# Kernel optimization log

Hardware: AMD Instinct MI355X
Metric: run time of the kernel (lower is better)

Reference implementation:

```python
import jax, jax.numpy as jnp
import numpy as np

N, T, D_KQ, E_KQ, D_V, E_V, H = 2, 2048, 1024, 1024, 1024, 1024, 16


def setup_inputs() -> dict:
    key = jax.random.key(0)
    ks = jax.random.split(key, 12)
    def lin(k, fan_in, fan_out):
        return jax.random.normal(k, (fan_in, fan_out), jnp.float32) * (1.0 / np.sqrt(fan_in))
    return {
        "kq": jax.random.normal(ks[0], (N, T, D_KQ), jnp.float32),
        "v": jax.random.normal(ks[1], (N, T, D_V), jnp.float32),
        "Wk": lin(ks[2], D_KQ, E_KQ), "bk": jnp.zeros((E_KQ,), jnp.float32),
        "Wq": lin(ks[3], D_KQ, E_KQ), "bq": jnp.zeros((E_KQ,), jnp.float32),
        "Wv": lin(ks[4], D_V, E_V),   "bv": jnp.zeros((E_V,), jnp.float32),
        "W1": lin(ks[5], E_V, 4 * E_V), "b1": jnp.zeros((4 * E_V,), jnp.float32),
        "W2": lin(ks[6], 4 * E_V, E_V), "b2": jnp.zeros((E_V,), jnp.float32),
    }


def _shifted_causal_mask(T):
    # triu(-inf, diagonal=0): block j >= i (strictly-past attention), except [0,0] unmasked
    row = jnp.arange(T)[:, None]
    col = jnp.arange(T)[None, :]
    mask = jnp.where(col < row, 0.0, -jnp.inf).astype(jnp.float32)
    return mask.at[0, 0].set(0.0)


def reference(kq, v, Wk, bk, Wq, bq, Wv, bv, W1, b1, W2, b2):
    n, T, _ = kq.shape
    hd_kq = E_KQ // H
    hd_v = E_V // H
    # projections -> [n, H, T, hd]
    k = (kq @ Wk + bk).reshape(n, T, H, hd_kq).transpose(0, 2, 1, 3)
    q = (kq @ Wq + bq).reshape(n, T, H, hd_kq).transpose(0, 2, 1, 3)
    vv = (v @ Wv + bv).reshape(n, T, H, hd_v).transpose(0, 2, 1, 3)
    # NOTE: no 1/sqrt(d) scaling, faithful to source
    scores = jnp.einsum("bhqd,bhkd->bhqk", q, k) + _shifted_causal_mask(T)
    attn = jax.nn.softmax(scores, axis=-1)
    out = jnp.einsum("bhqk,bhkd->bhqd", attn, vv)
    out = out.transpose(0, 2, 1, 3).reshape(n, T, E_V)
    # GELU FFN (torch nn.GELU default = exact erf form)
    h = jax.nn.gelu(out @ W1 + b1, approximate=False)
    return h @ W2 + b2
```

## Files before the change

kernel.cpp:

```cpp
#include <hip/hip_runtime.h>

typedef short bf16x8 __attribute__((ext_vector_type(8)));
typedef unsigned short u16x8 __attribute__((ext_vector_type(8)));
typedef float f32x4 __attribute__((ext_vector_type(4)));
typedef unsigned short u16;

#define MFMA16(a, b, c) __builtin_amdgcn_mfma_f32_16x16x32_bf16((a), (b), (c), 0, 0, 0)
#define VMCNT0() asm volatile("s_waitcnt vmcnt(0)" ::: "memory")
#define VMCNTN(n) asm volatile("s_waitcnt vmcnt(" #n ")" ::: "memory")

__device__ __forceinline__ u16 bf16_rtn(float f) {
  unsigned u = __float_as_uint(f);
  u += 0x7fffu + ((u >> 16) & 1u);
  return (u16)(u >> 16);
}
__device__ __forceinline__ float bf16_to_f(u16 h) {
  return __uint_as_float(((unsigned)h) << 16);
}
__device__ __forceinline__ void splitf(float f, u16& hi, u16& lo) {
  hi = bf16_rtn(f);
  lo = bf16_rtn(f - bf16_to_f(hi));
}
__device__ __forceinline__ void gload16(const void* g, void* l) {
  __builtin_amdgcn_global_load_lds(
      (const __attribute__((address_space(1))) unsigned int*)g,
      (__attribute__((address_space(3))) unsigned int*)l, 16, 0, 0);
}
__device__ __forceinline__ float exp2_hw(float x) {
  float r;
  asm("v_exp_f32 %0, %1" : "=v"(r) : "v"(x));
  return r;
}
__device__ __forceinline__ float gelu_t(float x) {
  float u = x * x;
  float z2 = x * fmaf(u, 0.10294407f, 2.30222726f);
  float den = exp2_hw(z2) + 1.0f;
  float s = __builtin_amdgcn_rcpf(den);
  return fmaf(-x, s, x);
}
__device__ __forceinline__ void swz_bid(int& bx, int& by) {
  int gx = gridDim.x;
  int lin = (int)blockIdx.y * gx + (int)blockIdx.x;
  int cpx = (gx * (int)gridDim.y) >> 3;
  int nl = (lin & 7) * cpx + (lin >> 3);
  bx = nl % gx;
  by = nl / gx;
}

__global__ void k_cvt(const float* __restrict__ a, const float* __restrict__ b,
                      u16* __restrict__ ah, u16* __restrict__ vb) {
  int i = blockIdx.x * blockDim.x + threadIdx.x;
  const int N4 = 1 << 20;
  const float4 v4 = (i < N4) ? ((const float4*)a)[i] : ((const float4*)b)[i - N4];
  ushort4 h;
  h.x = bf16_rtn(v4.x);
  h.y = bf16_rtn(v4.y);
  h.z = bf16_rtn(v4.z);
  h.w = bf16_rtn(v4.w);
  if (i < N4)
    ((ushort4*)ah)[i] = h;
  else
    ((ushort4*)vb)[i - N4] = h;
}

__global__ void k_tconvW(const float* __restrict__ Wk, const float* __restrict__ Wq,
                         const float* __restrict__ Wv, u16* __restrict__ hi,
                         u16* __restrict__ lo, u16* __restrict__ wvt) {
  int z = blockIdx.z;
  const float* in = (z == 0) ? Wk : (z == 1) ? Wq : Wv;
  __shared__ float tile[32][33];
  int c0 = blockIdx.x * 32, r0 = blockIdx.y * 32;
  int tx = threadIdx.x & 31, ty = threadIdx.x >> 5;
#pragma unroll
  for (int i = 0; i < 4; ++i)
    tile[ty + i * 8][tx] = in[(size_t)(r0 + ty + i * 8) * 1024 + c0 + tx];
  __syncthreads();
#pragma unroll
  for (int i = 0; i < 4; ++i) {
    float v = tile[tx][ty + i * 8];
    size_t o = (size_t)(c0 + ty + i * 8) * 1024 + r0 + tx;
    if (z < 2) {
      u16 h, l;
      splitf(v, h, l);
      hi[(size_t)z * 1048576 + o] = h;
      lo[(size_t)z * 1048576 + o] = l;
    } else {
      wvt[o] = bf16_rtn(v);
    }
  }
}

__global__ void k_tconv(const float* __restrict__ in, u16* __restrict__ hi,
                        int R, int C) {
  __shared__ float tile[32][33];
  int c0 = blockIdx.x * 32, r0 = blockIdx.y * 32;
  int tx = threadIdx.x & 31, ty = threadIdx.x >> 5;
#pragma unroll
  for (int i = 0; i < 4; ++i)
    tile[ty + i * 8][tx] = in[(size_t)(r0 + ty + i * 8) * C + c0 + tx];
  __syncthreads();
#pragma unroll
  for (int i = 0; i < 4; ++i)
    hi[(size_t)(c0 + ty + i * 8) * R + r0 + tx] = bf16_rtn(tile[tx][ty + i * 8]);
}

template <int GELU, int OUT, int BN>
__global__ __launch_bounds__(256) void k_gemm(
    const u16* __restrict__ A, const u16* __restrict__ B,
    const float* __restrict__ bias, void* __restrict__ C0,
    int M, int Nc, int K) {
  const int NB = BN / 32;
  const int BUFE = 8192 + BN * 64;
  __shared__ u16 sm[3 * BUFE];

  int bx, by;
  swz_bid(bx, by);
  int m0 = by * 128, n0 = bx * BN;
  int t = threadIdx.x, lane = t & 63, w = t >> 6;
  int wr = (w >> 1) * 64, wc = (w & 1) * (BN / 2);
  int li = lane & 15, g = lane >> 4;
  int lrow = lane >> 3, lcg = lane & 7;

  f32x4 acc[4][NB] = {};
  const int nk = K >> 6;

  auto stage = [&](int kb, int buf) {
    int k0 = kb * 64;
    u16* base = sm + buf * BUFE;
#pragma unroll
    for (int j = 0; j < 4; ++j) {
      int jj = w * 4 + j;
      int row = jj * 8 + lrow;
      int cg = lcg ^ (row & 7);
      gload16(A + (size_t)(m0 + row) * K + k0 + cg * 8, base + jj * 512);
    }
#pragma unroll
    for (int j = 0; j < NB; ++j) {
      int jj = w * NB + j;
      int row = jj * 8 + lrow;
      int cg = lcg ^ (row & 7);
      gload16(B + (size_t)(n0 + row) * K + k0 + cg * 8, base + 8192 + jj * 512);
    }
  };

  stage(0, 0);
  stage(1, 1);
  if (NB == 4) { VMCNTN(8); } else { VMCNTN(6); }
  __syncthreads();

  int cur = 0;
  for (int kb = 0; kb < nk; ++kb) {
    int stb = cur + 2;
    if (stb >= 3) stb -= 3;
    if (kb + 2 < nk) stage(kb + 2, stb);

    const u16* bs = sm + cur * BUFE;
#pragma unroll
    for (int kk = 0; kk < 2; ++kk) {
      bf16x8 af[4], bf[NB];
#pragma unroll
      for (int i = 0; i < 4; ++i) {
        int row = wr + i * 16 + li;
        af[i] = *(const bf16x8*)&bs[row * 64 + (((kk * 4 + g) ^ (li & 7)) << 3)];
      }
#pragma unroll
      for (int b = 0; b < NB; ++b) {
        int row = wc + b * 16 + li;
        bf[b] = *(const bf16x8*)&bs[8192 + row * 64 + (((kk * 4 + g) ^ (li & 7)) << 3)];
      }
#pragma unroll
      for (int a = 0; a < 4; ++a)
#pragma unroll
        for (int b = 0; b < NB; ++b) acc[a][b] = MFMA16(af[a], bf[b], acc[a][b]);
    }
    if (kb + 2 < nk) {
      if (NB == 4) { VMCNTN(8); } else { VMCNTN(6); }
    } else {
      VMCNT0();
    }
    __syncthreads();
    cur = (cur == 2) ? 0 : cur + 1;
  }

#pragma unroll
  for (int a = 0; a < 4; ++a)
#pragma unroll
    for (int b = 0; b < NB; ++b)
#pragma unroll
      for (int r = 0; r < 4; ++r) {
        int row = m0 + wr + a * 16 + g * 4 + r;
        int col = n0 + wc + b * 16 + li;
        float v = acc[a][b][r] + bias[col];
        if (GELU) v = gelu_t(v);
        if (OUT == 0) {
          ((float*)C0)[(size_t)row * Nc + col] = v;
        } else if (OUT == 1) {
          ((u16*)C0)[(size_t)row * Nc + col] = bf16_rtn(v);
        } else if (OUT == 5) {
          int nn = row >> 11, tt = row & 2047, kbb = tt >> 6, tr = tt & 63;
          int hq = col >> 6, d = col & 63;
          size_t base = (((size_t)nn * 16 + hq) * 32 + kbb) * 8192 + 4096;
          size_t ov = base + d * 64 + (tr & 7) + (((tr >> 3) ^ (d & 7)) << 3);
          ((u16*)C0)[ov] = bf16_rtn(v);
        }
      }
}

template <int GELU, int OUT>
__global__ __launch_bounds__(512, 1) void k_gemm2(
    const u16* __restrict__ A, const u16* __restrict__ B,
    const float* __restrict__ bias, void* __restrict__ C0,
    int M, int Nc, int K) {
  const int BUFE = 32768;
  __shared__ u16 sm[2 * BUFE];

  int bx, by;
  swz_bid(bx, by);
  int m0 = by * 256, n0 = bx * 256;
  int t = threadIdx.x, lane = t & 63, w = t >> 6;
  int wr = (w >> 2) * 128, wc = (w & 3) * 64;
  int li = lane & 15, g = lane >> 4;
  int lrow = lane >> 3, lcg = lane & 7;

  f32x4 acc[8][4] = {};
  const int nk = K >> 6;

  auto stage = [&](int kb, int buf) {
    int k0 = kb * 64;
    u16* base = sm + buf * BUFE;
#pragma unroll
    for (int j = 0; j < 4; ++j) {
      int jj = w * 4 + j;
      int row = jj * 8 + lrow;
      int cg = lcg ^ (row & 7);
      gload16(A + (size_t)(m0 + row) * K + k0 + cg * 8, base + jj * 512);
      gload16(B + (size_t)(n0 + row) * K + k0 + cg * 8, base + 16384 + jj * 512);
    }
  };

  stage(0, 0);
  VMCNT0();
  __syncthreads();

  int cur = 0;
  for (int kb = 0; kb < nk; ++kb) {
    if (kb + 1 < nk) stage(kb + 1, cur ^ 1);

    const u16* bs = sm + cur * BUFE;
#pragma unroll
    for (int kk = 0; kk < 2; ++kk) {
      bf16x8 af[8], bf[4];
#pragma unroll
      for (int i = 0; i < 8; ++i) {
        int row = wr + i * 16 + li;
        af[i] = *(const bf16x8*)&bs[row * 64 + (((kk * 4 + g) ^ (li & 7)) << 3)];
      }
#pragma unroll
      for (int b = 0; b < 4; ++b) {
        int row = wc + b * 16 + li;
        bf[b] = *(const bf16x8*)&bs[16384 + row * 64 + (((kk * 4 + g) ^ (li & 7)) << 3)];
      }
#pragma unroll
      for (int a = 0; a < 8; ++a)
#pragma unroll
        for (int b = 0; b < 4; ++b) acc[a][b] = MFMA16(af[a], bf[b], acc[a][b]);
    }
    VMCNT0();
    __syncthreads();
    cur ^= 1;
  }

#pragma unroll
  for (int a = 0; a < 8; ++a)
#pragma unroll
    for (int b = 0; b < 4; ++b)
#pragma unroll
      for (int r = 0; r < 4; ++r) {
        int row = m0 + wr + a * 16 + g * 4 + r;
        int col = n0 + wc + b * 16 + li;
        float v = acc[a][b][r] + bias[col];
        if (GELU) v = gelu_t(v);
        if (OUT == 1)
          ((u16*)C0)[(size_t)row * Nc + col] = bf16_rtn(v);
        else
          ((float*)C0)[(size_t)row * Nc + col] = v;
      }
}

__global__ __launch_bounds__(256) void k_gemm_s(
    const u16* __restrict__ Ahi, const u16* __restrict__ Bhi,
    const u16* __restrict__ Blo, const float* __restrict__ bias,
    const float* __restrict__ bias2, void* __restrict__ C0,
    void* __restrict__ C1, void* __restrict__ C2, int M, int Nc, int K) {
  const int BUFE = 12288;
  __shared__ u16 sm[3 * BUFE];

  int bx, by;
  swz_bid(bx, by);
  int m0 = by * 128, n0 = bx * 128;
  int t = threadIdx.x, lane = t & 63, w = t >> 6;
  int wr = (w >> 1) * 64, wc = (w & 1) * 64;
  int li = lane & 15, g = lane >> 4;
  int srow = lane >> 2;
  int sc = ((lane & 3) ^ ((srow >> 1) & 3)) * 8;

  f32x4 acc[4][4] = {};
  const int nk = K >> 5;

  auto stage = [&](int kb, int buf) {
    int k0 = kb * 32;
    u16* base = sm + buf * BUFE;
#pragma unroll
    for (int c = 0; c < 2; ++c) {
      int row = w * 32 + c * 16 + srow;
      int ldso = w * 1024 + c * 512;
      gload16(Ahi + (size_t)(m0 + row) * K + k0 + sc, base + ldso);
      gload16(Bhi + (size_t)(n0 + row) * K + k0 + sc, base + 4096 + ldso);
      gload16(Blo + (size_t)(n0 + row) * K + k0 + sc, base + 8192 + ldso);
    }
  };

  stage(0, 0);
  stage(1, 1);
  VMCNTN(6);
  __syncthreads();

  int cur = 0;
  for (int kb = 0; kb < nk; ++kb) {
    int stb = cur + 2;
    if (stb >= 3) stb -= 3;
    if (kb + 2 < nk) stage(kb + 2, stb);

    const u16* bs = sm + cur * BUFE;
    bf16x8 af[4], bfr[4], bfl[4];
#pragma unroll
    for (int i = 0; i < 4; ++i) {
      int swz = (g ^ ((li >> 1) & 3)) << 3;
      af[i] = *(const bf16x8*)&bs[(wr + i * 16 + li) * 32 + swz];
      bfr[i] = *(const bf16x8*)&bs[4096 + (wc + i * 16 + li) * 32 + swz];
      bfl[i] = *(const bf16x8*)&bs[8192 + (wc + i * 16 + li) * 32 + swz];
    }
#pragma unroll
    for (int a = 0; a < 4; ++a)
#pragma unroll
      for (int b = 0; b < 4; ++b) {
        acc[a][b] = MFMA16(af[a], bfr[b], acc[a][b]);
        acc[a][b] = MFMA16(af[a], bfl[b], acc[a][b]);
      }
    if (kb + 2 < nk) {
      VMCNTN(6);
    } else {
      VMCNT0();
    }
    __syncthreads();
    cur = (cur == 2) ? 0 : cur + 1;
  }

#pragma unroll
  for (int a = 0; a < 4; ++a)
#pragma unroll
    for (int b = 0; b < 4; ++b)
#pragma unroll
      for (int r = 0; r < 4; ++r) {
        int row = m0 + wr + a * 16 + g * 4 + r;
        int col = n0 + wc + b * 16 + li;
        float bb = col < 1024 ? bias[col] : bias2[col - 1024];
        float v = acc[a][b][r] + bb;
        if (col < 1024) {
          int nn = row >> 11, tt = row & 2047, kbb = tt >> 6, tr = tt & 63;
          int hq = col >> 6, d = col & 63, ks = d >> 5, dc = d & 31;
          size_t base = (((size_t)nn * 16 + hq) * 32 + kbb) * 8192;
          size_t oh = base + ks * 2048 + tr * 32 + (dc & 7) +
                      (((dc >> 3) ^ ((tr >> 1) & 3)) << 3);
          ((u16*)C0)[oh] = bf16_rtn(v);
        } else {
          int cq = col - 1024;
          float vq = v * 1.4426950408889634f;
          u16 hh, ll;
          splitf(vq, hh, ll);
          size_t off = (((size_t)(row >> 11) * 16 + (cq >> 6)) * 2048 + (row & 2047)) * 64 + (cq & 63);
          ((u16*)C1)[off] = hh;
          ((u16*)C2)[off] = ll;
        }
      }
}

__global__ __launch_bounds__(512) void k_attn(
    const u16* __restrict__ Qh, const u16* __restrict__ Ql,
    const u16* __restrict__ KV, u16* __restrict__ out) {
  const int T = 2048, HD = 64, H = 16, E = 1024;
  int hc = blockIdx.x;
  int h = hc & 15, n = hc >> 4;
  int qq = 15 - (int)blockIdx.y;
  __shared__ u16 KB[3][8192];
  __shared__ u16 P[2][128][36];
  int t = threadIdx.x, lane = t & 63, w = t >> 6;
  int li = lane & 15, g = lane >> 4;

  const size_t nh = (size_t)n * H + h;
  const u16* qhb = Qh + (nh * 2048 + (size_t)qq * 128) * 64;
  const u16* qlb = Ql + (nh * 2048 + (size_t)qq * 128) * 64;
  const u16* kvb = KV + nh * 32 * 8192;

  bf16x8 qh[2], ql[2];
#pragma unroll
  for (int ks = 0; ks < 2; ++ks) {
    qh[ks] = *(const bf16x8*)&qhb[(w * 16 + li) * 64 + ks * 32 + g * 8];
    ql[ks] = *(const bf16x8*)&qlb[(w * 16 + li) * 64 + ks * 32 + g * 8];
  }

#pragma unroll
  for (int j = 0; j < 2; ++j)
    gload16(kvb + (w * 2 + j) * 512 + lane * 8, &KB[0][(w * 2 + j) * 512]);
#pragma unroll
  for (int j = 0; j < 2; ++j)
    gload16(kvb + 8192 + (w * 2 + j) * 512 + lane * 8, &KB[1][(w * 2 + j) * 512]);
  VMCNTN(2);
  __syncthreads();

  float lr[4] = {0.f, 0.f, 0.f, 0.f};
  f32x4 O[4] = {};
  int cur = 0;
  const int nkb = 2 * qq + 2;

  for (int kb = 0; kb < nkb; ++kb) {
    int stb = cur + 2;
    if (stb >= 3) stb -= 3;
    if (kb + 2 < nkb) {
      const u16* src = kvb + (size_t)(kb + 2) * 8192 + (w * 2) * 512 + lane * 8;
#pragma unroll
      for (int j = 0; j < 2; ++j)
        gload16(src + j * 512, &KB[stb][(w * 2 + j) * 512]);
    }

    f32x4 s[4] = {};
#pragma unroll
    for (int ks = 0; ks < 2; ++ks)
#pragma unroll
      for (int c = 0; c < 4; ++c) {
        int jr = c * 16 + li;
        int sw = (jr >> 1) & 3;
        bf16x8 kh = *(const bf16x8*)&KB[cur][ks * 2048 + jr * 32 + ((g ^ sw) << 3)];
        s[c] = MFMA16(qh[ks], kh, s[c]);
        s[c] = MFMA16(ql[ks], kh, s[c]);
      }

    if (kb >= 2 * qq) {
#pragma unroll
      for (int c = 0; c < 4; ++c)
#pragma unroll
        for (int r = 0; r < 4; ++r) {
          int i = qq * 128 + w * 16 + g * 4 + r;
          int j = kb * 64 + c * 16 + li;
          if (!(j < i || (i == 0 && j == 0))) s[c][r] = -INFINITY;
        }
    }

#pragma unroll
    for (int c = 0; c < 4; ++c)
#pragma unroll
      for (int r = 0; r < 4; ++r) {
        float p = exp2_hw(s[c][r]);
        s[c][r] = p;
        lr[r] += p;
      }

#pragma unroll
    for (int c = 0; c < 4; ++c)
#pragma unroll
      for (int r = 0; r < 4; ++r)
        P[c >> 1][w * 16 + g * 4 + r][(c & 1) * 16 + li] = bf16_rtn(s[c][r]);

#pragma unroll
    for (int ks = 0; ks < 2; ++ks) {
      bf16x8 pa = *(const bf16x8*)&P[ks][w * 16 + li][g * 8];
#pragma unroll
      for (int c = 0; c < 4; ++c) {
        int d = c * 16 + li;
        int tc = ks * 4 + g;
        bf16x8 vb = *(const bf16x8*)&KB[cur][4096 + d * 64 + ((tc ^ (d & 7)) << 3)];
        O[c] = MFMA16(pa, vb, O[c]);
      }
    }
    if (kb + 2 < nkb) {
      VMCNTN(2);
    } else {
      VMCNT0();
    }
    __syncthreads();
    cur = (cur == 2) ? 0 : cur + 1;
  }

#pragma unroll
  for (int off = 1; off < 16; off <<= 1)
#pragma unroll
    for (int r = 0; r < 4; ++r) lr[r] += __shfl_xor(lr[r], off, 16);

#pragma unroll
  for (int c = 0; c < 4; ++c)
#pragma unroll
    for (int r = 0; r < 4; ++r) {
      float v = O[c][r] / lr[r];
      size_t row = (size_t)n * T + qq * 128 + w * 16 + g * 4 + r;
      out[row * E + h * HD + c * 16 + li] = bf16_rtn(v);
    }
}

extern "C" void kernel_launch(void* const* d_in, const int* in_sizes, int n_in,
                              void* d_out, int out_size, void* d_ws, size_t ws_size,
                              hipStream_t stream) {
  const float* kq = (const float*)d_in[0];
  const float* v = (const float*)d_in[1];
  const float* Wk = (const float*)d_in[2];
  const float* bk = (const float*)d_in[3];
  const float* Wq = (const float*)d_in[4];
  const float* bq = (const float*)d_in[5];
  const float* Wv = (const float*)d_in[6];
  const float* bv = (const float*)d_in[7];
  const float* W1 = (const float*)d_in[8];
  const float* b1 = (const float*)d_in[9];
  const float* W2 = (const float*)d_in[10];
  const float* b2 = (const float*)d_in[11];
  float* outp = (float*)d_out;

  char* ws = (char*)d_ws;
  u16* kq_hi = (u16*)(ws + 0);
  u16* v_bf = (u16*)(ws + 8388608);
  u16* hbuf = (u16*)(ws + 0);
  u16* WkqT_hi = (u16*)(ws + 33554432);
  u16* WkqT_lo = (u16*)(ws + 37748736);
  u16* WvT = (u16*)(ws + 41943040);
  u16* W1T = (u16*)(ws + 44040192);
  u16* W2T = (u16*)(ws + 52428800);
  u16* Qh = (u16*)(ws + 60817408);
  u16* Ql = (u16*)(ws + 69206016);
  u16* KV = (u16*)(ws + 77594624);
  u16* attn_o = (u16*)(ws + 102760448);

  k_cvt<<<8192, 256, 0, stream>>>(kq, v, kq_hi, v_bf);
  k_tconvW<<<dim3(32, 32, 3), 256, 0, stream>>>(Wk, Wq, Wv, WkqT_hi, WkqT_lo, WvT);
  k_tconv<<<dim3(128, 32), 256, 0, stream>>>(W1, W1T, 1024, 4096);
  k_tconv<<<dim3(32, 128), 256, 0, stream>>>(W2, W2T, 4096, 1024);

  k_gemm_s<<<dim3(16, 32), 256, 0, stream>>>(
      kq_hi, WkqT_hi, WkqT_lo, bk, bq, KV, Qh, Ql, 4096, 2048, 1024);
  k_gemm<0, 5, 64><<<dim3(16, 32), 256, 0, stream>>>(
      v_bf, WvT, bv, KV, 4096, 1024, 1024);

  k_attn<<<dim3(32, 16), 512, 0, stream>>>(Qh, Ql, KV, attn_o);

  k_gemm2<1, 1><<<dim3(16, 16), 512, 0, stream>>>(
      attn_o, W1T, b1, hbuf, 4096, 4096, 1024);
  k_gemm<0, 0, 128><<<dim3(8, 32), 256, 0, stream>>>(
      hbuf, W2T, b2, outp, 4096, 1024, 4096);
}
```

Before: 213.6 us.

## Pair causal query tiles per attention block and merge prep kernels

The attention kernel now processes two query tiles per block (qa=15-y and qb=y). This balances causal work across blocks and lets both tiles reuse each K/V tile loaded into LDS, halving the grid. The four conversion and transpose kernels are merged into a single k_prep launch to cut launch overhead. The cost is higher register and LDS use per attention block, which may reduce occupancy, and only 256 attention blocks remain to fill the device.

New measurement: 217.5 us. Within noise of the previous version (+1.8%).

```diff
diff --git a/kernel.cpp b/kernel.cpp
--- a/kernel.cpp
+++ b/kernel.cpp
@@ -47,61 +47,71 @@
   by = nl / gx;
 }
 
-__global__ void k_cvt(const float* __restrict__ a, const float* __restrict__ b,
-                      u16* __restrict__ ah, u16* __restrict__ vb) {
-  int i = blockIdx.x * blockDim.x + threadIdx.x;
-  const int N4 = 1 << 20;
-  const float4 v4 = (i < N4) ? ((const float4*)a)[i] : ((const float4*)b)[i - N4];
-  ushort4 h;
-  h.x = bf16_rtn(v4.x);
-  h.y = bf16_rtn(v4.y);
-  h.z = bf16_rtn(v4.z);
-  h.w = bf16_rtn(v4.w);
-  if (i < N4)
-    ((ushort4*)ah)[i] = h;
-  else
-    ((ushort4*)vb)[i - N4] = h;
-}
-
-__global__ void k_tconvW(const float* __restrict__ Wk, const float* __restrict__ Wq,
-                         const float* __restrict__ Wv, u16* __restrict__ hi,
-                         u16* __restrict__ lo, u16* __restrict__ wvt) {
-  int z = blockIdx.z;
-  const float* in = (z == 0) ? Wk : (z == 1) ? Wq : Wv;
+__global__ void k_prep(const float* __restrict__ kq, const float* __restrict__ v,
+                       const float* __restrict__ Wk, const float* __restrict__ Wq,
+                       const float* __restrict__ Wv, const float* __restrict__ W1,
+                       const float* __restrict__ W2, u16* __restrict__ kq_hi,
+                       u16* __restrict__ v_bf, u16* __restrict__ WkqT_hi,
+                       u16* __restrict__ WkqT_lo, u16* __restrict__ WvT,
+                       u16* __restrict__ W1T, u16* __restrict__ W2T) {
   __shared__ float tile[32][33];
-  int c0 = blockIdx.x * 32, r0 = blockIdx.y * 32;
+  int bid = blockIdx.x;
+  if (bid < 8192) {
+    int i = bid * 256 + threadIdx.x;
+    const int N4 = 1 << 20;
+    const float4 v4 = (i < N4) ? ((const float4*)kq)[i] : ((const float4*)v)[i - N4];
+    ushort4 h;
+    h.x = bf16_rtn(v4.x);
+    h.y = bf16_rtn(v4.y);
+    h.z = bf16_rtn(v4.z);
+    h.w = bf16_rtn(v4.w);
+    if (i < N4)
+      ((ushort4*)kq_hi)[i] = h;
+    else
+      ((ushort4*)v_bf)[i - N4] = h;
+    return;
+  }
   int tx = threadIdx.x & 31, ty = threadIdx.x >> 5;
-#pragma unroll
-  for (int i = 0; i < 4; ++i)
-    tile[ty + i * 8][tx] = in[(size_t)(r0 + ty + i * 8) * 1024 + c0 + tx];
-  __syncthreads();
-#pragma unroll
-  for (int i = 0; i < 4; ++i) {
-    float v = tile[tx][ty + i * 8];
-    size_t o = (size_t)(c0 + ty + i * 8) * 1024 + r0 + tx;
-    if (z < 2) {
-      u16 h, l;
-      splitf(v, h, l);
-      hi[(size_t)z * 1048576 + o] = h;
-      lo[(size_t)z * 1048576 + o] = l;
-    } else {
-      wvt[o] = bf16_rtn(v);
-    }
+  if (bid < 11264) {
+    int zz = bid - 8192;
+    int z = zz >> 10, rem = zz & 1023;
+    int bx = rem & 31, byy = rem >> 5;
+    const float* in = (z == 0) ? Wk : (z == 1) ? Wq : Wv;
+    int c0 = bx * 32, r0 = byy * 32;
+#pragma unroll
+    for (int i = 0; i < 4; ++i)
+      tile[ty + i * 8][tx] = in[(size_t)(r0 + ty + i * 8) * 1024 + c0 + tx];
+    __syncthreads();
+#pragma unroll
+    for (int i = 0; i < 4; ++i) {
+      float vv = tile[tx][ty + i * 8];
+      size_t o = (size_t)(c0 + ty + i * 8) * 1024 + r0 + tx;
+      if (z < 2) {
+        u16 h, l;
+        splitf(vv, h, l);
+        WkqT_hi[(size_t)z * 1048576 + o] = h;
+        WkqT_lo[(size_t)z * 1048576 + o] = l;
+      } else {
+        WvT[o] = bf16_rtn(vv);
+      }
+    }
+    return;
   }
-}
-
-__global__ void k_tconv(const float* __restrict__ in, u16* __restrict__ hi,
-                        int R, int C) {
-  __shared__ float tile[32][33];
-  int c0 = blockIdx.x * 32, r0 = blockIdx.y * 32;
-  int tx = threadIdx.x & 31, ty = threadIdx.x >> 5;
+  int zz = bid - 11264;
+  int z = zz >> 12, rem = zz & 4095;
+  const float* in = z ? W2 : W1;
+  u16* outp = z ? W2T : W1T;
+  int R = z ? 4096 : 1024, C = z ? 1024 : 4096;
+  int bx = z ? (rem & 31) : (rem & 127);
+  int byy = z ? (rem >> 5) : (rem >> 7);
+  int c0 = bx * 32, r0 = byy * 32;
 #pragma unroll
   for (int i = 0; i < 4; ++i)
     tile[ty + i * 8][tx] = in[(size_t)(r0 + ty + i * 8) * C + c0 + tx];
   __syncthreads();
 #pragma unroll
   for (int i = 0; i < 4; ++i)
-    hi[(size_t)(c0 + ty + i * 8) * R + r0 + tx] = bf16_rtn(tile[tx][ty + i * 8]);
+    outp[(size_t)(c0 + ty + i * 8) * R + r0 + tx] = bf16_rtn(tile[tx][ty + i * 8]);
 }
 
 template <int GELU, int OUT, int BN>
@@ -391,22 +401,28 @@
   const int T = 2048, HD = 64, H = 16, E = 1024;
   int hc = blockIdx.x;
   int h = hc & 15, n = hc >> 4;
-  int qq = 15 - (int)blockIdx.y;
+  int y = blockIdx.y;
+  int qa = 15 - y, qb = y;
   __shared__ u16 KB[3][8192];
-  __shared__ u16 P[2][128][36];
+  __shared__ u16 Pa[2][128][36];
+  __shared__ u16 Pb[2][128][36];
   int t = threadIdx.x, lane = t & 63, w = t >> 6;
   int li = lane & 15, g = lane >> 4;
 
   const size_t nh = (size_t)n * H + h;
-  const u16* qhb = Qh + (nh * 2048 + (size_t)qq * 128) * 64;
-  const u16* qlb = Ql + (nh * 2048 + (size_t)qq * 128) * 64;
+  const u16* qhbA = Qh + (nh * 2048 + (size_t)qa * 128) * 64;
+  const u16* qlbA = Ql + (nh * 2048 + (size_t)qa * 128) * 64;
+  const u16* qhbB = Qh + (nh * 2048 + (size_t)qb * 128) * 64;
+  const u16* qlbB = Ql + (nh * 2048 + (size_t)qb * 128) * 64;
   const u16* kvb = KV + nh * 32 * 8192;
 
-  bf16x8 qh[2], ql[2];
+  bf16x8 qhA[2], qlA[2], qhB[2], qlB[2];
 #pragma unroll
   for (int ks = 0; ks < 2; ++ks) {
-    qh[ks] = *(const bf16x8*)&qhb[(w * 16 + li) * 64 + ks * 32 + g * 8];
-    ql[ks] = *(const bf16x8*)&qlb[(w * 16 + li) * 64 + ks * 32 + g * 8];
+    qhA[ks] = *(const bf16x8*)&qhbA[(w * 16 + li) * 64 + ks * 32 + g * 8];
+    qlA[ks] = *(const bf16x8*)&qlbA[(w * 16 + li) * 64 + ks * 32 + g * 8];
+    qhB[ks] = *(const bf16x8*)&qhbB[(w * 16 + li) * 64 + ks * 32 + g * 8];
+    qlB[ks] = *(const bf16x8*)&qlbB[(w * 16 + li) * 64 + ks * 32 + g * 8];
   }
 
 #pragma unroll
@@ -418,10 +434,11 @@
   VMCNTN(2);
   __syncthreads();
 
-  float lr[4] = {0.f, 0.f, 0.f, 0.f};
-  f32x4 O[4] = {};
+  float lra[4] = {0.f, 0.f, 0.f, 0.f}, lrb[4] = {0.f, 0.f, 0.f, 0.f};
+  f32x4 Oa[4] = {}, Ob[4] = {};
   int cur = 0;
-  const int nkb = 2 * qq + 2;
+  const int nkb = 2 * qa + 2;
+  const int nkbB = 2 * qb + 2;
 
   for (int kb = 0; kb < nkb; ++kb) {
     int stb = cur + 2;
@@ -432,54 +449,88 @@
       for (int j = 0; j < 2; ++j)
         gload16(src + j * 512, &KB[stb][(w * 2 + j) * 512]);
     }
-
-    f32x4 s[4] = {};
+    bool actB = kb < nkbB;
+
+    bf16x8 khf[2][4];
 #pragma unroll
     for (int ks = 0; ks < 2; ++ks)
 #pragma unroll
       for (int c = 0; c < 4; ++c) {
         int jr = c * 16 + li;
         int sw = (jr >> 1) & 3;
-        bf16x8 kh = *(const bf16x8*)&KB[cur][ks * 2048 + jr * 32 + ((g ^ sw) << 3)];
-        s[c] = MFMA16(qh[ks], kh, s[c]);
-        s[c] = MFMA16(ql[ks], kh, s[c]);
-      }
-
-    if (kb >= 2 * qq) {
+        khf[ks][c] = *(const bf16x8*)&KB[cur][ks * 2048 + jr * 32 + ((g ^ sw) << 3)];
+      }
+
+    f32x4 sa[4] = {}, sb[4] = {};
+#pragma unroll
+    for (int ks = 0; ks < 2; ++ks)
+#pragma unroll
+      for (int c = 0; c < 4; ++c) {
+        sa[c] = MFMA16(qhA[ks], khf[ks][c], sa[c]);
+        sa[c] = MFMA16(qlA[ks], khf[ks][c], sa[c]);
+      }
+    if (actB) {
+#pragma unroll
+      for (int ks = 0; ks < 2; ++ks)
+#pragma unroll
+        for (int c = 0; c < 4; ++c) {
+          sb[c] = MFMA16(qhB[ks], khf[ks][c], sb[c]);
+          sb[c] = MFMA16(qlB[ks], khf[ks][c], sb[c]);
+        }
+    }
+
+    if (kb >= 2 * qa) {
 #pragma unroll
       for (int c = 0; c < 4; ++c)
 #pragma unroll
         for (int r = 0; r < 4; ++r) {
-          int i = qq * 128 + w * 16 + g * 4 + r;
+          int i = qa * 128 + w * 16 + g * 4 + r;
           int j = kb * 64 + c * 16 + li;
-          if (!(j < i || (i == 0 && j == 0))) s[c][r] = -INFINITY;
+          if (!(j < i || (i == 0 && j == 0))) sa[c][r] = -INFINITY;
         }
     }
+    if (actB && kb >= 2 * qb) {
+#pragma unroll
+      for (int c = 0; c < 4; ++c)
+#pragma unroll
+        for (int r = 0; r < 4; ++r) {
+          int i = qb * 128 + w * 16 + g * 4 + r;
+          int j = kb * 64 + c * 16 + li;
+          if (!(j < i || (i == 0 && j == 0))) sb[c][r] = -INFINITY;
+        }
+    }
 
 #pragma unroll
     for (int c = 0; c < 4; ++c)
 #pragma unroll
       for (int r = 0; r < 4; ++r) {
-        float p = exp2_hw(s[c][r]);
-        s[c][r] = p;
-        lr[r] += p;
-      }
-
-#pragma unroll
-    for (int c = 0; c < 4; ++c)
-#pragma unroll
-      for (int r = 0; r < 4; ++r)
-        P[c >> 1][w * 16 + g * 4 + r][(c & 1) * 16 + li] = bf16_rtn(s[c][r]);
+        float p = exp2_hw(sa[c][r]);
+        lra[r] += p;
+        Pa[c >> 1][w * 16 + g * 4 + r][(c & 1) * 16 + li] = bf16_rtn(p);
+      }
+    if (actB) {
+#pragma unroll
+      for (int c = 0; c < 4; ++c)
+#pragma unroll
+        for (int r = 0; r < 4; ++r) {
+          float p = exp2_hw(sb[c][r]);
+          lrb[r] += p;
+          Pb[c >> 1][w * 16 + g * 4 + r][(c & 1) * 16 + li] = bf16_rtn(p);
+        }
+    }
 
 #pragma unroll
     for (int ks = 0; ks < 2; ++ks) {
-      bf16x8 pa = *(const bf16x8*)&P[ks][w * 16 + li][g * 8];
+      bf16x8 paA = *(const bf16x8*)&Pa[ks][w * 16 + li][g * 8];
+      bf16x8 paB;
+      if (actB) paB = *(const bf16x8*)&Pb[ks][w * 16 + li][g * 8];
 #pragma unroll
       for (int c = 0; c < 4; ++c) {
         int d = c * 16 + li;
         int tc = ks * 4 + g;
         bf16x8 vb = *(const bf16x8*)&KB[cur][4096 + d * 64 + ((tc ^ (d & 7)) << 3)];
-        O[c] = MFMA16(pa, vb, O[c]);
+        Oa[c] = MFMA16(paA, vb, Oa[c]);
+        if (actB) Ob[c] = MFMA16(paB, vb, Ob[c]);
       }
     }
     if (kb + 2 < nkb) {
@@ -494,15 +545,19 @@
 #pragma unroll
   for (int off = 1; off < 16; off <<= 1)
 #pragma unroll
-    for (int r = 0; r < 4; ++r) lr[r] += __shfl_xor(lr[r], off, 16);
+    for (int r = 0; r < 4; ++r) {
+      lra[r] += __shfl_xor(lra[r], off, 16);
+      lrb[r] += __shfl_xor(lrb[r], off, 16);
+    }
 
 #pragma unroll
   for (int c = 0; c < 4; ++c)
 #pragma unroll
     for (int r = 0; r < 4; ++r) {
-      float v = O[c][r] / lr[r];
-      size_t row = (size_t)n * T + qq * 128 + w * 16 + g * 4 + r;
-      out[row * E + h * HD + c * 16 + li] = bf16_rtn(v);
+      size_t rowA = (size_t)n * T + qa * 128 + w * 16 + g * 4 + r;
+      out[rowA * E + h * HD + c * 16 + li] = bf16_rtn(Oa[c][r] / lra[r]);
+      size_t rowB = (size_t)n * T + qb * 128 + w * 16 + g * 4 + r;
+      out[rowB * E + h * HD + c * 16 + li] = bf16_rtn(Ob[c][r] / lrb[r]);
     }
 }
 
@@ -537,17 +592,15 @@
   u16* KV = (u16*)(ws + 77594624);
   u16* attn_o = (u16*)(ws + 102760448);
 
-  k_cvt<<<8192, 256, 0, stream>>>(kq, v, kq_hi, v_bf);
-  k_tconvW<<<dim3(32, 32, 3), 256, 0, stream>>>(Wk, Wq, Wv, WkqT_hi, WkqT_lo, WvT);
-  k_tconv<<<dim3(128, 32), 256, 0, stream>>>(W1, W1T, 1024, 4096);
-  k_tconv<<<dim3(32, 128), 256, 0, stream>>>(W2, W2T, 4096, 1024);
+  k_prep<<<19456, 256, 0, stream>>>(kq, v, Wk, Wq, Wv, W1, W2, kq_hi, v_bf,
+                                    WkqT_hi, WkqT_lo, WvT, W1T, W2T);
 
   k_gemm_s<<<dim3(16, 32), 256, 0, stream>>>(
       kq_hi, WkqT_hi, WkqT_lo, bk, bq, KV, Qh, Ql, 4096, 2048, 1024);
   k_gemm<0, 5, 64><<<dim3(16, 32), 256, 0, stream>>>(
       v_bf, WvT, bv, KV, 4096, 1024, 1024);
 
-  k_attn<<<dim3(32, 16), 512, 0, stream>>>(Qh, Ql, KV, attn_o);
+  k_attn<<<dim3(32, 8), 512, 0, stream>>>(Qh, Ql, KV, attn_o);
 
   k_gemm2<1, 1><<<dim3(16, 16), 512, 0, stream>>>(
       attn_o, W1T, b1, hbuf, 4096, 4096, 1024);
```
